# Kernel optimization log

Measured on AMD Instinct MI355X. Metric: run time of the kernel, lower is better.

Reference implementation:

```python
import jax, jax.numpy as jnp
import numpy as np
from jax import lax

B, C, H, W = 64, 256, 64, 64
RED = 16


def setup_inputs() -> dict:
    key = jax.random.key(0)
    k1, k2, k3, k4, k5 = jax.random.split(key, 5)
    x = jax.random.normal(k1, (B, C, H, W), dtype=jnp.float32)
    # conv1: Conv2d(C, 1, kernel_size=1) -> weight (1,C,1,1) stored squeezed as (C,), bias scalar
    conv_w = jax.random.normal(k2, (C,), dtype=jnp.float32) * (1.0 / np.sqrt(C))
    conv_b = jax.random.normal(k3, (1,), dtype=jnp.float32) * 0.01
    # SE MLP: Linear(C, C//RED, bias=False), Linear(C//RED, C, bias=False)
    fc1_w = jax.random.normal(k4, (C // RED, C), dtype=jnp.float32) * (1.0 / np.sqrt(C))
    fc2_w = jax.random.normal(k5, (C, C // RED), dtype=jnp.float32) * (1.0 / np.sqrt(C // RED))
    return {"x": x, "conv_w": conv_w, "conv_b": conv_b, "fc1_w": fc1_w, "fc2_w": fc2_w}


def reference(x, conv_w, conv_b, fc1_w, fc2_w):
    b, c, h, w = x.shape
    # --- spatial_pool ---
    # group batch into chunks of 8, pool over (group, H, W) with 3x3x3 avg, stride 1, pad 1
    g = x.reshape(b // 8, 8, c, h, w).transpose(0, 2, 1, 3, 4)  # (G, C, 8, H, W)
    summed = lax.reduce_window(
        g, 0.0, lax.add,
        window_dimensions=(1, 1, 3, 3, 3),
        window_strides=(1, 1, 1, 1, 1),
        padding=[(0, 0), (0, 0), (1, 1), (1, 1), (1, 1)],
    )
    pooled = summed / 27.0  # AvgPool3d(3,1,1) with count_include_pad=True
    pooled = pooled.transpose(0, 2, 1, 3, 4).reshape(b, c, h, w)
    # 1x1 conv C -> 1
    logits = jnp.einsum('bchw,c->bhw', pooled, conv_w) + conv_b[0]  # (B,H,W)
    attn = jax.nn.softmax(logits.reshape(b, h * w), axis=-1)  # softmax over spatial positions
    # softmax-weighted spatial pooling of the ORIGINAL x
    y = jnp.einsum('bcs,bs->bc', x.reshape(b, c, h * w), attn)  # (B,C)
    # --- SE gating MLP ---
    hid = jax.nn.relu(y @ fc1_w.T)           # (B, C//RED)
    gate = jax.nn.sigmoid(hid @ fc2_w.T)     # (B, C)
    return x * gate[:, :, None, None]
```

## Files before the change

kernel.cpp:

```cpp
#include <hip/hip_runtime.h>
#include <math.h>

#define B 64
#define C 256
#define S 4096
#define S4 1024

__global__ __launch_bounds__(256) void k1_chanreduce(const float4* __restrict__ x4,
                                                     const float* __restrict__ cw,
                                                     float4* __restrict__ t4) {
    __shared__ float wl[C];
    const int tid = threadIdx.x;
    wl[tid] = cw[tid];
    __syncthreads();
    const int b = blockIdx.x >> 2;
    const int chunk = blockIdx.x & 3;
    const int s4 = chunk * 256 + tid;
    const float4* xb = x4 + (size_t)b * C * S4 + s4;
    float4 acc = make_float4(0.f, 0.f, 0.f, 0.f);
#pragma unroll 8
    for (int c = 0; c < C; ++c) {
        float4 v = xb[(size_t)c * S4];
        float w = wl[c];
        acc.x += v.x * w; acc.y += v.y * w; acc.z += v.z * w; acc.w += v.w * w;
    }
    t4[b * S4 + s4] = acc;
}

__global__ __launch_bounds__(256) void k2_pool_softmax(const float* __restrict__ t,
                                                       const float* __restrict__ cb,
                                                       float* __restrict__ attn) {
    __shared__ float ts[S];
    __shared__ float rs[S];
    __shared__ float red[16];
    const int b = blockIdx.x;
    const int d = b & 7;
    const int tid = threadIdx.x;
    const float* t0 = t + (size_t)b * S;

    for (int k = 0; k < 16; ++k) {
        int s = k * 256 + tid;
        float v = t0[s];
        if (d > 0) v += t0[s - S];
        if (d < 7) v += t0[s + S];
        ts[s] = v;
    }
    __syncthreads();
    for (int k = 0; k < 16; ++k) {
        int s = k * 256 + tid;
        int w = s & 63;
        float v = ts[s];
        if (w > 0)  v += ts[s - 1];
        if (w < 63) v += ts[s + 1];
        rs[s] = v;
    }
    __syncthreads();
    const float bias = cb[0];
    float l[16];
    float m = -INFINITY;
    for (int k = 0; k < 16; ++k) {
        int s = k * 256 + tid;
        float v = rs[s];
        if (s >= 64)     v += rs[s - 64];
        if (s < S - 64)  v += rs[s + 64];
        l[k] = v * (1.0f / 27.0f) + bias;
        m = fmaxf(m, l[k]);
    }
    for (int o = 32; o > 0; o >>= 1) m = fmaxf(m, __shfl_xor(m, o));
    const int wave = tid >> 6;
    if ((tid & 63) == 0) red[wave] = m;
    __syncthreads();
    if (tid == 0) {
        float mm = red[0];
        for (int i = 1; i < 4; ++i) mm = fmaxf(mm, red[i]);
        red[8] = mm;
    }
    __syncthreads();
    m = red[8];
    float sum = 0.f;
    for (int k = 0; k < 16; ++k) { l[k] = expf(l[k] - m); sum += l[k]; }
    for (int o = 32; o > 0; o >>= 1) sum += __shfl_xor(sum, o);
    if ((tid & 63) == 0) red[wave] = sum;
    __syncthreads();
    if (tid == 0) {
        float ss = red[0] + red[1] + red[2] + red[3];
        red[9] = 1.0f / ss;
    }
    __syncthreads();
    const float inv = red[9];
    float* ab = attn + (size_t)b * S;
    for (int k = 0; k < 16; ++k) {
        int s = k * 256 + tid;
        ab[s] = l[k] * inv;
    }
}

__global__ __launch_bounds__(256) void k3_weighted_pool(const float4* __restrict__ x4,
                                                        const float4* __restrict__ attn4,
                                                        float* __restrict__ y) {
    __shared__ float4 al[S4];
    const int tid = threadIdx.x;
    const int b = blockIdx.x >> 6;
    const int cg = blockIdx.x & 63;
    for (int k = 0; k < 4; ++k) {
        int i = k * 256 + tid;
        al[i] = attn4[(size_t)b * S4 + i];
    }
    __syncthreads();
    const int c = cg * 4 + (tid >> 6);
    const int lane = tid & 63;
    const float4* xb = x4 + ((size_t)(b * C + c)) * S4;
    float acc = 0.f;
#pragma unroll 4
    for (int it = 0; it < 16; ++it) {
        int s4 = it * 64 + lane;
        float4 xv = xb[s4];
        float4 av = al[s4];
        acc += xv.x * av.x + xv.y * av.y + xv.z * av.z + xv.w * av.w;
    }
    for (int o = 32; o > 0; o >>= 1) acc += __shfl_xor(acc, o);
    if (lane == 0) y[b * C + c] = acc;
}

__global__ __launch_bounds__(256) void k4_mlp(const float* __restrict__ y,
                                              const float* __restrict__ fc1,
                                              const float* __restrict__ fc2,
                                              float* __restrict__ gate) {
    __shared__ float yl[C];
    __shared__ float ph[16][17];
    __shared__ float hid[16];
    const int b = blockIdx.x;
    const int tid = threadIdx.x;
    yl[tid] = y[(size_t)b * C + tid];
    __syncthreads();
    const int j = tid >> 4, part = tid & 15;
    float p = 0.f;
#pragma unroll
    for (int k = 0; k < 16; ++k) {
        int cc = part + k * 16;
        p += yl[cc] * fc1[j * C + cc];
    }
    ph[j][part] = p;
    __syncthreads();
    if (tid < 16) {
        float s = 0.f;
#pragma unroll
        for (int k = 0; k < 16; ++k) s += ph[tid][k];
        hid[tid] = fmaxf(s, 0.f);
    }
    __syncthreads();
    float g = 0.f;
#pragma unroll
    for (int jj = 0; jj < 16; ++jj) g += hid[jj] * fc2[tid * 16 + jj];
    gate[(size_t)b * C + tid] = 1.0f / (1.0f + expf(-g));
}

__global__ __launch_bounds__(256) void k5_scale(const float4* __restrict__ x4,
                                               const float* __restrict__ gate,
                                               float4* __restrict__ out4) {
    const size_t total = (size_t)B * C * S4;
    size_t i = (size_t)blockIdx.x * 256 + threadIdx.x;
    const size_t stride = (size_t)gridDim.x * 256;
    for (; i < total; i += stride) {
        int bc = (int)(i >> 10);
        float g = gate[bc];
        float4 v = x4[i];
        v.x *= g; v.y *= g; v.z *= g; v.w *= g;
        out4[i] = v;
    }
}

extern "C" void kernel_launch(void* const* d_in, const int* in_sizes, int n_in,
                              void* d_out, int out_size, void* d_ws, size_t ws_size,
                              hipStream_t stream) {
    const float* x   = (const float*)d_in[0];
    const float* cw  = (const float*)d_in[1];
    const float* cb  = (const float*)d_in[2];
    const float* fc1 = (const float*)d_in[3];
    const float* fc2 = (const float*)d_in[4];
    float* out = (float*)d_out;

    float* t    = (float*)d_ws;
    float* attn = t + (size_t)B * S;
    float* y    = attn + (size_t)B * S;
    float* gate = y + (size_t)B * C;

    k1_chanreduce<<<256, 256, 0, stream>>>((const float4*)x, cw, (float4*)t);
    k2_pool_softmax<<<B, 256, 0, stream>>>(t, cb, attn);
    k3_weighted_pool<<<B * 64, 256, 0, stream>>>((const float4*)x, (const float4*)attn, y);
    k4_mlp<<<B, 256, 0, stream>>>(y, fc1, fc2, gate);
    k5_scale<<<4096, 256, 0, stream>>>((const float4*)x, gate, (float4*)out);
}
```

Measured before the change: 546.7 us.

## Split channel reduction across groups, drop attn LDS staging, nontemporal scale

The channel-weighted reduction is split into 4 channel groups, giving 1024 blocks instead of 256 so more CUs can stream x. Each group writes its own partial sums, and the pool/softmax kernel adds them up. The weighted-pool kernel now reads attention straight from global memory (L2/cache) instead of staging it in LDS, which removes a sync. The scale kernel uses a fixed unrolled loop with nontemporal loads and stores to avoid polluting the cache. The costs are more workspace and extra partial reads in k2.

```diff
diff --git a/kernel.cpp b/kernel.cpp
--- a/kernel.cpp
+++ b/kernel.cpp
@@ -5,29 +5,35 @@
 #define C 256
 #define S 4096
 #define S4 1024
+#define NG 4
+#define CPG 64
+
+typedef float v4f __attribute__((ext_vector_type(4)));
 
 __global__ __launch_bounds__(256) void k1_chanreduce(const float4* __restrict__ x4,
                                                      const float* __restrict__ cw,
-                                                     float4* __restrict__ t4) {
-    __shared__ float wl[C];
+                                                     float4* __restrict__ tp4) {
+    __shared__ float wl[CPG];
     const int tid = threadIdx.x;
-    wl[tid] = cw[tid];
+    const int bid = blockIdx.x;
+    const int b = bid >> 4;
+    const int cg = (bid >> 2) & (NG - 1);
+    const int chunk = bid & 3;
+    if (tid < CPG) wl[tid] = cw[cg * CPG + tid];
     __syncthreads();
-    const int b = blockIdx.x >> 2;
-    const int chunk = blockIdx.x & 3;
     const int s4 = chunk * 256 + tid;
-    const float4* xb = x4 + (size_t)b * C * S4 + s4;
+    const float4* xb = x4 + (size_t)b * C * S4 + (size_t)cg * CPG * S4 + s4;
     float4 acc = make_float4(0.f, 0.f, 0.f, 0.f);
 #pragma unroll 8
-    for (int c = 0; c < C; ++c) {
+    for (int c = 0; c < CPG; ++c) {
         float4 v = xb[(size_t)c * S4];
         float w = wl[c];
         acc.x += v.x * w; acc.y += v.y * w; acc.z += v.z * w; acc.w += v.w * w;
     }
-    t4[b * S4 + s4] = acc;
+    tp4[((size_t)cg * B + b) * S4 + s4] = acc;
 }
 
-__global__ __launch_bounds__(256) void k2_pool_softmax(const float* __restrict__ t,
+__global__ __launch_bounds__(256) void k2_pool_softmax(const float* __restrict__ tp,
                                                        const float* __restrict__ cb,
                                                        float* __restrict__ attn) {
     __shared__ float ts[S];
@@ -36,13 +42,18 @@
     const int b = blockIdx.x;
     const int d = b & 7;
     const int tid = threadIdx.x;
-    const float* t0 = t + (size_t)b * S;
 
     for (int k = 0; k < 16; ++k) {
         int s = k * 256 + tid;
-        float v = t0[s];
-        if (d > 0) v += t0[s - S];
-        if (d < 7) v += t0[s + S];
+        float v = 0.f;
+#pragma unroll
+        for (int g = 0; g < NG; ++g) {
+            const float* t0 = tp + ((size_t)g * B + b) * S + s;
+            float u = t0[0];
+            if (d > 0) u += t0[-S];
+            if (d < 7) u += t0[S];
+            v += u;
+        }
         ts[s] = v;
     }
     __syncthreads();
@@ -98,26 +109,22 @@
 __global__ __launch_bounds__(256) void k3_weighted_pool(const float4* __restrict__ x4,
                                                         const float4* __restrict__ attn4,
                                                         float* __restrict__ y) {
-    __shared__ float4 al[S4];
     const int tid = threadIdx.x;
     const int b = blockIdx.x >> 6;
     const int cg = blockIdx.x & 63;
-    for (int k = 0; k < 4; ++k) {
-        int i = k * 256 + tid;
-        al[i] = attn4[(size_t)b * S4 + i];
-    }
-    __syncthreads();
     const int c = cg * 4 + (tid >> 6);
     const int lane = tid & 63;
     const float4* xb = x4 + ((size_t)(b * C + c)) * S4;
+    const float4* ab = attn4 + (size_t)b * S4;
     float acc = 0.f;
 #pragma unroll 4
     for (int it = 0; it < 16; ++it) {
         int s4 = it * 64 + lane;
         float4 xv = xb[s4];
-        float4 av = al[s4];
+        float4 av = ab[s4];
         acc += xv.x * av.x + xv.y * av.y + xv.z * av.z + xv.w * av.w;
     }
+#pragma unroll
     for (int o = 32; o > 0; o >>= 1) acc += __shfl_xor(acc, o);
     if (lane == 0) y[b * C + c] = acc;
 }
@@ -155,18 +162,17 @@
     gate[(size_t)b * C + tid] = 1.0f / (1.0f + expf(-g));
 }
 
-__global__ __launch_bounds__(256) void k5_scale(const float4* __restrict__ x4,
+__global__ __launch_bounds__(256) void k5_scale(const v4f* __restrict__ x4,
                                                const float* __restrict__ gate,
-                                               float4* __restrict__ out4) {
-    const size_t total = (size_t)B * C * S4;
+                                               v4f* __restrict__ out4) {
     size_t i = (size_t)blockIdx.x * 256 + threadIdx.x;
-    const size_t stride = (size_t)gridDim.x * 256;
-    for (; i < total; i += stride) {
-        int bc = (int)(i >> 10);
-        float g = gate[bc];
-        float4 v = x4[i];
-        v.x *= g; v.y *= g; v.z *= g; v.w *= g;
-        out4[i] = v;
+    const size_t stride = (size_t)4096 * 256;
+#pragma unroll 4
+    for (int it = 0; it < 16; ++it, i += stride) {
+        float g = gate[(int)(i >> 10)];
+        v4f v = __builtin_nontemporal_load(&x4[i]);
+        v *= g;
+        __builtin_nontemporal_store(v, &out4[i]);
     }
 }
 
@@ -180,14 +186,14 @@
     const float* fc2 = (const float*)d_in[4];
     float* out = (float*)d_out;
 
-    float* t    = (float*)d_ws;
-    float* attn = t + (size_t)B * S;
+    float* tp   = (float*)d_ws;
+    float* attn = tp + (size_t)NG * B * S;
     float* y    = attn + (size_t)B * S;
     float* gate = y + (size_t)B * C;
 
-    k1_chanreduce<<<256, 256, 0, stream>>>((const float4*)x, cw, (float4*)t);
-    k2_pool_softmax<<<B, 256, 0, stream>>>(t, cb, attn);
+    k1_chanreduce<<<B * NG * 4, 256, 0, stream>>>((const float4*)x, cw, (float4*)tp);
+    k2_pool_softmax<<<B, 256, 0, stream>>>(tp, cb, attn);
     k3_weighted_pool<<<B * 64, 256, 0, stream>>>((const float4*)x, (const float4*)attn, y);
     k4_mlp<<<B, 256, 0, stream>>>(y, fc1, fc2, gate);
-    k5_scale<<<4096, 256, 0, stream>>>((const float4*)x, gate, (float4*)out);
+    k5_scale<<<4096, 256, 0, stream>>>((const v4f*)x, gate, (v4f*)out);
 }
```

New measurement: 554.1 us. About the same (+1.4%).
